# Kernel optimization log

Measured on AMD Instinct MI355X. Metric: run time of the kernel, lower is better.

The kernel has to match this reference:

```python
import jax, jax.numpy as jnp
import numpy as np

DIM = 1024
HEADS = 16
HEAD_DIM = DIM // HEADS
FFN = 4 * DIM
EPS = 1e-5


def layer_norm(x, g, b):
    mu = jnp.mean(x, axis=-1, keepdims=True)
    var = jnp.mean(jnp.square(x - mu), axis=-1, keepdims=True)
    return (x - mu) * jax.lax.rsqrt(var + EPS) * g + b


def setup_inputs() -> dict:
    key = jax.random.key(0)
    ks = jax.random.split(key, 12)
    s_d = 1.0 / np.sqrt(DIM)
    s_f = 1.0 / np.sqrt(FFN)
    return {
        "x": jax.random.normal(ks[0], (2, 2048, DIM), dtype=jnp.float32),
        "ln1_g": jnp.ones((DIM,), jnp.float32),
        "ln1_b": jnp.zeros((DIM,), jnp.float32),
        "q_w": jax.random.normal(ks[1], (DIM, DIM), jnp.float32) * s_d,
        "k_w": jax.random.normal(ks[2], (DIM, DIM), jnp.float32) * s_d,
        "v_w": jax.random.normal(ks[3], (DIM, DIM), jnp.float32) * s_d,
        "o_w": jax.random.normal(ks[4], (DIM, DIM), jnp.float32) * s_d,
        "ln2_g": jnp.ones((DIM,), jnp.float32),
        "ln2_b": jnp.zeros((DIM,), jnp.float32),
        "ffn_in_w": jax.random.normal(ks[5], (FFN, DIM), jnp.float32) * s_d,
        "ffn_in_b": jnp.zeros((FFN,), jnp.float32),
        "sw_w": jax.random.normal(ks[6], (FFN, FFN), jnp.float32) * s_f,
        "sw_v": jax.random.normal(ks[7], (FFN, FFN), jnp.float32) * s_f,
        "ffn_out_w": jax.random.normal(ks[8], (DIM, FFN), jnp.float32) * s_f,
        "ffn_out_b": jnp.zeros((DIM,), jnp.float32),
    }


def reference(x, ln1_g, ln1_b, q_w, k_w, v_w, o_w, ln2_g, ln2_b,
              ffn_in_w, ffn_in_b, sw_w, sw_v, ffn_out_w, ffn_out_b):
    B, L, D = x.shape
    scale = HEAD_DIM ** -0.5

    # --- attention block ---
    h = layer_norm(x, ln1_g, ln1_b)
    q = (h @ q_w.T).reshape(B, L, HEADS, HEAD_DIM).transpose(0, 2, 1, 3)
    k = (h @ k_w.T).reshape(B, L, HEADS, HEAD_DIM).transpose(0, 2, 1, 3)
    v = (h @ v_w.T).reshape(B, L, HEADS, HEAD_DIM).transpose(0, 2, 1, 3)
    attn = jnp.einsum("bhqd,bhkd->bhqk", q, k) * scale
    attn = jax.nn.softmax(attn, axis=-1)
    out = jnp.einsum("bhqk,bhkd->bhqd", attn, v)
    out = out.transpose(0, 2, 1, 3).reshape(B, L, D)
    x = x + out @ o_w.T

    # --- FFN block: Linear -> SwiGLU -> Linear ---
    h = layer_norm(x, ln2_g, ln2_b)
    u = h @ ffn_in_w.T + ffn_in_b                 # [B,L,FFN]
    g = jax.nn.silu(u @ sw_w.T) * (u @ sw_v.T)    # SwiGLU
    x = x + g @ ffn_out_w.T + ffn_out_b
    return x
```

## Files before the change

kernel.cpp:

```cpp
#include <hip/hip_runtime.h>
#include <hip/hip_bf16.h>

#define TOK 4096
#define DIM 1024
#define FFN_N 4096
#define SEQ 2048
#define HD 64
#define QKS 3072

using short8 = __attribute__((ext_vector_type(8))) short;
using short4v = __attribute__((ext_vector_type(4))) short;
using f32x4 = __attribute__((ext_vector_type(4))) float;

__device__ __forceinline__ short f2b(float f){
  return __builtin_bit_cast(short, __float2bfloat16(f));
}
__device__ __forceinline__ float b2f(short s){
  return __bfloat162float(__builtin_bit_cast(__hip_bfloat16, s));
}
__device__ __forceinline__ unsigned cvtpk(float lo, float hi){
  unsigned r;
  asm("v_cvt_pk_bf16_f32 %0, %1, %2" : "=v"(r) : "v"(lo), "v"(hi));
  return r;
}

__device__ __forceinline__ void gl_lds16(const short* g, short* l){
  __builtin_amdgcn_global_load_lds(
      (const __attribute__((address_space(1))) unsigned int*)g,
      (__attribute__((address_space(3))) unsigned int*)l, 16, 0, 0);
}

#define BARRAW() asm volatile("s_barrier" ::: "memory")
#define VMCNT(n) asm volatile("s_waitcnt vmcnt(" #n ")" ::: "memory")

__global__ __launch_bounds__(256) void castk(const float* __restrict__ src,
                                             short* __restrict__ dst, int n){
  int stride = gridDim.x*256*4;
  for (int i = (blockIdx.x*256 + threadIdx.x)*4; i < n; i += stride){
    float4 v = *reinterpret_cast<const float4*>(src + i);
    short4v o; o[0]=f2b(v.x); o[1]=f2b(v.y); o[2]=f2b(v.z); o[3]=f2b(v.w);
    *reinterpret_cast<short4v*>(dst + i) = o;
  }
}

__global__ __launch_bounds__(256) void lnk(const float* __restrict__ x,
                                           const float* __restrict__ g,
                                           const float* __restrict__ b,
                                           short* __restrict__ out){
  int row = blockIdx.x;
  int t = threadIdx.x;
  const float* xr = x + (size_t)row*DIM;
  float4 v = *reinterpret_cast<const float4*>(xr + t*4);
  float s = v.x+v.y+v.z+v.w;
  float s2 = v.x*v.x+v.y*v.y+v.z*v.z+v.w*v.w;
  #pragma unroll
  for (int off=1; off<64; off<<=1){ s += __shfl_xor(s,off); s2 += __shfl_xor(s2,off); }
  __shared__ float as_[4], as2_[4];
  if ((t&63)==0){ as_[t>>6]=s; as2_[t>>6]=s2; }
  __syncthreads();
  s = as_[0]+as_[1]+as_[2]+as_[3];
  s2 = as2_[0]+as2_[1]+as2_[2]+as2_[3];
  float mu = s * (1.0f/DIM);
  float var = s2 * (1.0f/DIM) - mu*mu;
  float r = rsqrtf(var + 1e-5f);
  float4 gv = *reinterpret_cast<const float4*>(g + t*4);
  float4 bv = *reinterpret_cast<const float4*>(b + t*4);
  short4v o;
  o[0]=f2b((v.x-mu)*r*gv.x + bv.x);
  o[1]=f2b((v.y-mu)*r*gv.y + bv.y);
  o[2]=f2b((v.z-mu)*r*gv.z + bv.z);
  o[3]=f2b((v.w-mu)*r*gv.w + bv.w);
  *reinterpret_cast<short4v*>(out + (size_t)row*DIM + t*4) = o;
}

template<int MODE>
__global__ __launch_bounds__(256,2) void gemm_bt(
    const short* __restrict__ A, const short* __restrict__ Bt,
    short* __restrict__ Cb, float* __restrict__ Cf,
    const float* __restrict__ bias, const float* __restrict__ resid,
    const short* __restrict__ aux,
    int M, int N, int K)
{
  __shared__ __align__(16) short Al[128*32];
  __shared__ __align__(16) short Bl[128*32];
  const int tid = threadIdx.x, lane = tid & 63, w = tid >> 6;
  const int wr = w >> 1, wc = w & 1;
  const int bx = blockIdx.x, by = blockIdx.y;

  const short* ga0 = A  + (size_t)(by*128 + w*32 + (lane>>2))*K + (lane&3)*8;
  const short* gb0 = Bt + (size_t)(bx*128 + w*32 + (lane>>2))*K + (lane&3)*8;
  short* la0 = &Al[w*32*32];
  short* lb0 = &Bl[w*32*32];

  f32x4 acc[4][4] = {};

  for (int k0 = 0; k0 < K; k0 += 32){
    __syncthreads();
    gl_lds16(ga0 + k0,                 la0);
    gl_lds16(ga0 + k0 + (size_t)16*K,  la0 + 16*32);
    gl_lds16(gb0 + k0,                 lb0);
    gl_lds16(gb0 + k0 + (size_t)16*K,  lb0 + 16*32);
    __syncthreads();
    short8 af[4], bf[4];
    #pragma unroll
    for (int m=0;m<4;m++)
      af[m] = *reinterpret_cast<const short8*>(&Al[(wr*64 + m*16 + (lane&15))*32 + (lane>>4)*8]);
    #pragma unroll
    for (int n=0;n<4;n++)
      bf[n] = *reinterpret_cast<const short8*>(&Bl[(wc*64 + n*16 + (lane&15))*32 + (lane>>4)*8]);
    #pragma unroll
    for (int m=0;m<4;m++)
      #pragma unroll
      for (int n=0;n<4;n++)
        acc[m][n] = __builtin_amdgcn_mfma_f32_16x16x32_bf16(af[m], bf[n], acc[m][n], 0,0,0);
  }

  #pragma unroll
  for (int m=0;m<4;m++){
    #pragma unroll
    for (int n=0;n<4;n++){
      #pragma unroll
      for (int j=0;j<4;j++){
        int r = by*128 + wr*64 + m*16 + ((lane>>4)<<2) + j;
        int c = bx*128 + wc*64 + n*16 + (lane&15);
        float v = acc[m][n][j];
        if (MODE==1 || MODE==3) v += bias[c];
        size_t idx = (size_t)r*N + c;
        if (MODE==4){
          float a = b2f(aux[idx]);
          float sg = a / (1.0f + __expf(-a));
          Cb[idx] = f2b(sg * v);
        } else if (MODE<=1) {
          Cb[idx] = f2b(v);
        } else {
          Cf[idx] = resid[idx] + v;
        }
      }
    }
  }
}

template<int MODE>
__global__ __launch_bounds__(512,2) void gemm256(
    const short* __restrict__ A, const short* __restrict__ Bt,
    short* __restrict__ Cb,
    const float* __restrict__ bias, const short* __restrict__ aux,
    int M, int N, int K)
{
  __shared__ __align__(16) short L[65536];
  const int tid = threadIdx.x, lane = tid&63, w = tid>>6;
  const int q15 = lane&15, h8 = lane>>4;
  const int wm = w>>2, wn = w&3;
  const int NT = K>>6;

  int bid = blockIdx.x;
  int wg = (bid&7)*(gridDim.x>>3) + (bid>>3);
  const int by = wg >> 4, bx = wg & 15;

  const int isub = w*8 + (lane>>3);
  const int koff = ((lane&7) ^ ((lane>>3)&7))*8;

  const short* gA[2][2]; const short* gB[2][2];
  #pragma unroll
  for (int hh=0; hh<2; hh++){
    #pragma unroll
    for (int j=0; j<2; j++){
      int i = j*64 + isub;
      int Ra = by*256 + (i>>6)*128 + hh*64 + (i&63);
      gA[hh][j] = A + (size_t)Ra*K + koff;
      int Rb = bx*256 + (i>>5)*64 + hh*32 + (i&31);
      gB[hh][j] = Bt + (size_t)Rb*K + koff;
    }
  }

  auto stA = [&](int db, int hh, int j, int kt){
    gl_lds16(gA[hh][j] + (size_t)kt*64, &L[db*32768 + hh*8192 + j*4096 + w*512]);
  };
  auto stB = [&](int db, int hh, int j, int kt){
    gl_lds16(gB[hh][j] + (size_t)kt*64, &L[db*32768 + (2+hh)*8192 + j*4096 + w*512]);
  };
  auto rdA = [&](int db, int mh, int m, int ks)->short8{
    int i = wm*64 + m*16 + q15;
    int ch = (ks*4 + h8) ^ (i&7);
    return *reinterpret_cast<const short8*>(&L[db*32768 + mh*8192 + i*64 + ch*8]);
  };
  auto rdB = [&](int db, int nh, int n, int ks)->short8{
    int i = wn*32 + n*16 + q15;
    int ch = (ks*4 + h8) ^ (i&7);
    return *reinterpret_cast<const short8*>(&L[db*32768 + (2+nh)*8192 + i*64 + ch*8]);
  };

  f32x4 acc[8][4] = {};
  short8 af[4][2], bf0[2][2], bf1[2][2];

#define MFMA_QUAD(MH, NH, BF)                                                  \
  __builtin_amdgcn_s_setprio(1);                                               \
  _Pragma("unroll")                                                            \
  for (int m=0;m<4;m++){                                                       \
    _Pragma("unroll")                                                          \
    for (int n=0;n<2;n++){                                                     \
      acc[(MH)*4+m][(NH)*2+n] = __builtin_amdgcn_mfma_f32_16x16x32_bf16(       \
          af[m][0], BF[n][0], acc[(MH)*4+m][(NH)*2+n], 0,0,0);                 \
      acc[(MH)*4+m][(NH)*2+n] = __builtin_amdgcn_mfma_f32_16x16x32_bf16(       \
          af[m][1], BF[n][1], acc[(MH)*4+m][(NH)*2+n], 0,0,0);                 \
    }                                                                          \
  }                                                                            \
  __builtin_amdgcn_s_setprio(0);

  stA(0,0,0,0); stA(0,0,1,0);
  stB(0,0,0,0); stB(0,0,1,0);
  stA(0,1,0,0); stA(0,1,1,0);
  stB(0,1,0,0); stB(0,1,1,0);
  VMCNT(4);
  BARRAW();

  for (int t = 0; t < NT; ++t){
    const int db = t&1;
    const bool pf = (t+1 < NT);

    #pragma unroll
    for (int m=0;m<4;m++){ af[m][0]=rdA(db,0,m,0); af[m][1]=rdA(db,0,m,1); }
    #pragma unroll
    for (int n=0;n<2;n++){ bf0[n][0]=rdB(db,0,n,0); bf0[n][1]=rdB(db,0,n,1); }
    if (pf){ stA(db^1,0,0,t+1); stA(db^1,0,1,t+1);
             stB(db^1,0,0,t+1); stB(db^1,0,1,t+1); }
    MFMA_QUAD(0,0,bf0);

    if (pf){ VMCNT(4); } else { VMCNT(0); }
    BARRAW();

    #pragma unroll
    for (int n=0;n<2;n++){ bf1[n][0]=rdB(db,1,n,0); bf1[n][1]=rdB(db,1,n,1); }
    if (pf){ stA(db^1,1,0,t+1); stA(db^1,1,1,t+1);
             stB(db^1,1,0,t+1); stB(db^1,1,1,t+1); }
    MFMA_QUAD(0,1,bf1);

    #pragma unroll
    for (int m=0;m<4;m++){ af[m][0]=rdA(db,1,m,0); af[m][1]=rdA(db,1,m,1); }
    MFMA_QUAD(1,1,bf1);
    MFMA_QUAD(1,0,bf0);

    if (pf){ VMCNT(4); }
    BARRAW();
  }

  #pragma unroll
  for (int mq=0;mq<8;mq++){
    #pragma unroll
    for (int nq=0;nq<4;nq++){
      #pragma unroll
      for (int jj=0;jj<4;jj++){
        int r = by*256 + wm*128 + mq*16 + h8*4 + jj;
        int c = bx*256 + wn*64  + nq*16 + q15;
        float v = acc[mq][nq][jj];
        if (MODE==1) v += bias[c];
        size_t idx = (size_t)r*N + c;
        if (MODE==4){
          float a = b2f(aux[idx]);
          float sg = a / (1.0f + __expf(-a));
          Cb[idx] = f2b(sg * v);
        } else {
          Cb[idx] = f2b(v);
        }
      }
    }
  }
#undef MFMA_QUAD
}

__global__ __launch_bounds__(256) void vtrk(const short* __restrict__ V,
                                            short* __restrict__ Vt){
  __shared__ __align__(16) short T[64*72];
  const int tid = threadIdx.x;
  const int bh = blockIdx.y;
  const int b = bh >> 4, hd = bh & 15;
  const int t0 = blockIdx.x * 64;
  const short* src = V + (size_t)b*SEQ*QKS + (size_t)hd*HD;

  const int r = tid>>2, c = tid&3;
  short8 a0 = *reinterpret_cast<const short8*>(src + (size_t)(t0+r)*QKS + c*8);
  short8 a1 = *reinterpret_cast<const short8*>(src + (size_t)(t0+r)*QKS + (c+4)*8);
  *reinterpret_cast<short8*>(&T[r*72 + c*8]) = a0;
  *reinterpret_cast<short8*>(&T[r*72 + (c+4)*8]) = a1;
  __syncthreads();

  short* dst = Vt + (size_t)bh*HD*SEQ;
  #pragma unroll
  for (int dd=0; dd<2; dd++){
    int d = (tid>>3) + dd*32;
    int tc = tid&7;
    short8 o;
    #pragma unroll
    for (int j=0;j<8;j++) o[j] = T[(tc*8+j)*72 + d];
    *reinterpret_cast<short8*>(dst + (size_t)d*SEQ + t0 + tc*8) = o;
  }
}

__global__ __launch_bounds__(256) void attnk(
    const short* __restrict__ Q, const short* __restrict__ K,
    const short* __restrict__ Vt, short* __restrict__ O)
{
  __shared__ __align__(16) short Kl[64*64];
  __shared__ __align__(16) short Vl[64*64];
  __shared__ __align__(16) short Pl[4*16*72];

  const int tid = threadIdx.x, lane = tid&63, w = tid>>6;
  const int h = lane>>4, q15 = lane&15;
  const int bh = blockIdx.y;
  const int b = bh >> 4, hd = bh & 15;
  const int q0 = blockIdx.x * 64;
  const size_t base  = (size_t)b*SEQ*QKS + (size_t)hd*HD;
  const size_t obase = (size_t)b*SEQ*DIM + (size_t)hd*HD;
  const size_t vbase = (size_t)bh*HD*SEQ;

  short8 aq[2];
  {
    int qrow = q0 + w*16 + q15;
    const short* qp = Q + base + (size_t)qrow*QKS + h*8;
    aq[0] = *reinterpret_cast<const short8*>(qp);
    aq[1] = *reinterpret_cast<const short8*>(qp + 32);
  }

  float mrun = -1e30f, lrun = 0.f;
  f32x4 o[4] = {};

  const int ksub = lane>>3;
  const int kchunk = (lane&7) ^ ksub;
  const short* kg0 = K + base + (size_t)(w*16 + ksub)*QKS + kchunk*8;
  const short* kg1 = kg0 + (size_t)8*QKS;
  const short* vg0 = Vt + vbase + (size_t)(w*16 + ksub)*SEQ + kchunk*8;
  const short* vg1 = vg0 + (size_t)8*SEQ;
  short* kl0 = &Kl[(w*16)*64];
  short* kl1 = &Kl[(w*16 + 8)*64];
  short* vl0 = &Vl[(w*16)*64];
  short* vl1 = &Vl[(w*16 + 8)*64];

  short* plw = &Pl[w*16*72];
  const int xk = (q15&7);

  for (int kv0 = 0; kv0 < SEQ; kv0 += 64){
    __syncthreads();
    gl_lds16(kg0 + (size_t)kv0*QKS, kl0);
    gl_lds16(kg1 + (size_t)kv0*QKS, kl1);
    gl_lds16(vg0 + kv0, vl0);
    gl_lds16(vg1 + kv0, vl1);
    __syncthreads();

    f32x4 s[4];
    #pragma unroll
    for (int nt=0; nt<4; nt++){
      const short8 kf0 = *reinterpret_cast<const short8*>(
          &Kl[(nt*16+q15)*64 + ((h    ^ xk)*8)]);
      const short8 kf1 = *reinterpret_cast<const short8*>(
          &Kl[(nt*16+q15)*64 + (((4+h)^ xk)*8)]);
      f32x4 t = {};
      t = __builtin_amdgcn_mfma_f32_16x16x32_bf16(kf0, aq[0], t, 0,0,0);
      t = __builtin_amdgcn_mfma_f32_16x16x32_bf16(kf1, aq[1], t, 0,0,0);
      s[nt] = t * 0.125f;
    }

    float pm = s[0][0];
    #pragma unroll
    for (int nt=0; nt<4; nt++)
      #pragma unroll
      for (int j=0; j<4; j++) pm = fmaxf(pm, s[nt][j]);
    pm = fmaxf(pm, __shfl_xor(pm, 16));
    pm = fmaxf(pm, __shfl_xor(pm, 32));

    float mn = fmaxf(mrun, pm);
    float al = __expf(mrun - mn);
    mrun = mn;
    float rs = 0.f;
    #pragma unroll
    for (int nt=0; nt<4; nt++)
      #pragma unroll
      for (int j=0; j<4; j++){
        s[nt][j] = __expf(s[nt][j] - mn);
        rs += s[nt][j];
      }
    rs += __shfl_xor(rs, 16);
    rs += __shfl_xor(rs, 32);
    lrun = lrun*al + rs;

    float alj[4];
    #pragma unroll
    for (int j=0;j<4;j++) alj[j] = __shfl(al, 4*h + j);
    #pragma unroll
    for (int dt=0;dt<4;dt++)
      #pragma unroll
      for (int j=0;j<4;j++) o[dt][j] *= alj[j];

    #pragma unroll
    for (int nt=0;nt<4;nt++){
      uint2 u;
      u.x = cvtpk(s[nt][0], s[nt][1]);
      u.y = cvtpk(s[nt][2], s[nt][3]);
      *reinterpret_cast<uint2*>(&plw[q15*72 + nt*16 + 4*h]) = u;
    }
    asm volatile("s_waitcnt lgkmcnt(0)" ::: "memory");
    const short8 ap0 = *reinterpret_cast<const short8*>(&plw[q15*72 +      h*8]);
    const short8 ap1 = *reinterpret_cast<const short8*>(&plw[q15*72 + 32 + h*8]);

    #pragma unroll
    for (int dt=0;dt<4;dt++){
      const short8 vf0 = *reinterpret_cast<const short8*>(
          &Vl[(dt*16+q15)*64 + ((h    ^ xk)*8)]);
      const short8 vf1 = *reinterpret_cast<const short8*>(
          &Vl[(dt*16+q15)*64 + (((4+h)^ xk)*8)]);
      o[dt] = __builtin_amdgcn_mfma_f32_16x16x32_bf16(ap0, vf0, o[dt], 0,0,0);
      o[dt] = __builtin_amdgcn_mfma_f32_16x16x32_bf16(ap1, vf1, o[dt], 0,0,0);
    }
  }

  float rl[4];
  #pragma unroll
  for (int j=0;j<4;j++) rl[j] = 1.0f / __shfl(lrun, 4*h + j);
  #pragma unroll
  for (int dt=0;dt<4;dt++)
    #pragma unroll
    for (int j=0;j<4;j++){
      int qrow = q0 + w*16 + 4*h + j;
      O[obase + (size_t)qrow*DIM + dt*16 + q15] = f2b(o[dt][j]*rl[j]);
    }
}

extern "C" void kernel_launch(void* const* d_in, const int* in_sizes, int n_in,
                              void* d_out, int out_size, void* d_ws, size_t ws_size,
                              hipStream_t stream) {
  const float* x     = (const float*)d_in[0];
  const float* ln1_g = (const float*)d_in[1];
  const float* ln1_b = (const float*)d_in[2];
  const float* q_w   = (const float*)d_in[3];
  const float* k_w   = (const float*)d_in[4];
  const float* v_w   = (const float*)d_in[5];
  const float* o_w   = (const float*)d_in[6];
  const float* ln2_g = (const float*)d_in[7];
  const float* ln2_b = (const float*)d_in[8];
  const float* fi_w  = (const float*)d_in[9];
  const float* fi_b  = (const float*)d_in[10];
  const float* sw_w  = (const float*)d_in[11];
  const float* sw_v  = (const float*)d_in[12];
  const float* fo_w  = (const float*)d_in[13];
  const float* fo_b  = (const float*)d_in[14];
  float* out = (float*)d_out;

  char* W = (char*)d_ws;
  const size_t MB = 1024*1024;
  short* qkvw = (short*)(W +   0*MB);
  short* ow   = (short*)(W +   6*MB);
  short* fiw  = (short*)(W +   8*MB);
  short* sww  = (short*)(W +  16*MB);
  short* swv  = (short*)(W +  48*MB);
  short* fow  = (short*)(W +  80*MB);
  short* hb   = (short*)(W +  88*MB);
  short* qkv  = (short*)(W +  96*MB);
  short* ab   = (short*)(W + 120*MB);
  float* x2   = (float*)(W + 128*MB);
  short* ub   = (short*)(W + 144*MB);
  short* gb   = (short*)(W + 176*MB);
  short* a1   = (short*)(W +  96*MB);
  short* vt   = (short*)(W + 144*MB);

  dim3 blk(256);
  castk<<<1024,blk,0,stream>>>(q_w, qkvw,             1024*1024);
  castk<<<1024,blk,0,stream>>>(k_w, qkvw + 1024*1024, 1024*1024);
  castk<<<1024,blk,0,stream>>>(v_w, qkvw + 2048*1024, 1024*1024);
  castk<<<1024,blk,0,stream>>>(o_w, ow, 1024*1024);
  castk<<<2048,blk,0,stream>>>(fi_w, fiw, 4096*1024);
  castk<<<2048,blk,0,stream>>>(sw_w, sww, 4096*4096);
  castk<<<2048,blk,0,stream>>>(sw_v, swv, 4096*4096);
  castk<<<2048,blk,0,stream>>>(fo_w, fow, 1024*4096);

  lnk<<<TOK,blk,0,stream>>>(x, ln1_g, ln1_b, hb);
  gemm_bt<0><<<dim3(24,32),blk,0,stream>>>(hb, qkvw, qkv, nullptr, nullptr, nullptr, nullptr, TOK, QKS, DIM);
  vtrk<<<dim3(SEQ/64,32),blk,0,stream>>>(qkv + 2048, vt);
  attnk<<<dim3(32,32),blk,0,stream>>>(qkv, qkv + 1024, vt, ab);
  gemm_bt<2><<<dim3(8,32),blk,0,stream>>>(ab, ow, nullptr, x2, nullptr, x, nullptr, TOK, DIM, DIM);
  lnk<<<TOK,blk,0,stream>>>(x2, ln2_g, ln2_b, hb);
  gemm256<1><<<256, 512, 0, stream>>>(hb, fiw, ub, fi_b, nullptr, TOK, FFN_N, DIM);
  gemm256<0><<<256, 512, 0, stream>>>(ub, sww, a1, nullptr, nullptr, TOK, FFN_N, FFN_N);
  gemm256<4><<<256, 512, 0, stream>>>(ub, swv, gb, nullptr, a1, TOK, FFN_N, FFN_N);
  gemm_bt<3><<<dim3(8,32),blk,0,stream>>>(gb, fow, nullptr, out, fo_b, x2, nullptr, TOK, DIM, FFN_N);
}
```

Measured before the change: 574.4 us.

## Double-buffer K/V tiles in attention with 128-key blocks and prefetch

The attention kernel now loads 128-key K/V tiles into double-buffered LDS and prefetches the next tile while computing the current one, which halves the barrier count per key. The V transpose kernel writes its output pre-swizzled so the direct global-to-LDS copy lands in the layout the MFMA reads expect. The aim is to hide global load latency behind MFMA and softmax work. In exchange, LDS use grows to about 64KB per block, which may cut occupancy.

```diff
diff --git a/kernel.cpp b/kernel.cpp
--- a/kernel.cpp
+++ b/kernel.cpp
@@ -292,16 +292,16 @@
     short8 o;
     #pragma unroll
     for (int j=0;j<8;j++) o[j] = T[(tc*8+j)*72 + d];
-    *reinterpret_cast<short8*>(dst + (size_t)d*SEQ + t0 + tc*8) = o;
+    *reinterpret_cast<short8*>(dst + (size_t)d*SEQ + t0 + ((tc ^ (d&7))*8)) = o;
   }
 }
 
 __global__ __launch_bounds__(256) void attnk(
     const short* __restrict__ Q, const short* __restrict__ K,
-    const short* __restrict__ Vt, short* __restrict__ O)
+    const short* __restrict__ Vp, short* __restrict__ O)
 {
-  __shared__ __align__(16) short Kl[64*64];
-  __shared__ __align__(16) short Vl[64*64];
+  __shared__ __align__(16) short Kb[2][128*64];
+  __shared__ __align__(16) short Vb[2][64*128];
   __shared__ __align__(16) short Pl[4*16*72];
 
   const int tid = threadIdx.x, lane = tid&63, w = tid>>6;
@@ -324,92 +324,104 @@
   float mrun = -1e30f, lrun = 0.f;
   f32x4 o[4] = {};
 
-  const int ksub = lane>>3;
-  const int kchunk = (lane&7) ^ ksub;
-  const short* kg0 = K + base + (size_t)(w*16 + ksub)*QKS + kchunk*8;
-  const short* kg1 = kg0 + (size_t)8*QKS;
-  const short* vg0 = Vt + vbase + (size_t)(w*16 + ksub)*SEQ + kchunk*8;
-  const short* vg1 = vg0 + (size_t)8*SEQ;
-  short* kl0 = &Kl[(w*16)*64];
-  short* kl1 = &Kl[(w*16 + 8)*64];
-  short* vl0 = &Vl[(w*16)*64];
-  short* vl1 = &Vl[(w*16 + 8)*64];
+  const short* kgp0 = K + base + (size_t)(w*32 + (lane>>3))*QKS
+                        + ((lane&7) ^ ((lane>>3)&7))*8;
+  const short* vgp0 = Vp + vbase + (size_t)(w*16 + (lane>>4))*SEQ + (lane&15)*8;
 
   short* plw = &Pl[w*16*72];
   const int xk = (q15&7);
 
-  for (int kv0 = 0; kv0 < SEQ; kv0 += 64){
-    __syncthreads();
-    gl_lds16(kg0 + (size_t)kv0*QKS, kl0);
-    gl_lds16(kg1 + (size_t)kv0*QKS, kl1);
-    gl_lds16(vg0 + kv0, vl0);
-    gl_lds16(vg1 + kv0, vl1);
-    __syncthreads();
-
-    f32x4 s[4];
-    #pragma unroll
-    for (int nt=0; nt<4; nt++){
-      const short8 kf0 = *reinterpret_cast<const short8*>(
-          &Kl[(nt*16+q15)*64 + ((h    ^ xk)*8)]);
-      const short8 kf1 = *reinterpret_cast<const short8*>(
-          &Kl[(nt*16+q15)*64 + (((4+h)^ xk)*8)]);
-      f32x4 t = {};
-      t = __builtin_amdgcn_mfma_f32_16x16x32_bf16(kf0, aq[0], t, 0,0,0);
-      t = __builtin_amdgcn_mfma_f32_16x16x32_bf16(kf1, aq[1], t, 0,0,0);
-      s[nt] = t * 0.125f;
-    }
-
-    float pm = s[0][0];
-    #pragma unroll
-    for (int nt=0; nt<4; nt++)
-      #pragma unroll
-      for (int j=0; j<4; j++) pm = fmaxf(pm, s[nt][j]);
-    pm = fmaxf(pm, __shfl_xor(pm, 16));
-    pm = fmaxf(pm, __shfl_xor(pm, 32));
-
-    float mn = fmaxf(mrun, pm);
-    float al = __expf(mrun - mn);
-    mrun = mn;
-    float rs = 0.f;
-    #pragma unroll
-    for (int nt=0; nt<4; nt++)
-      #pragma unroll
-      for (int j=0; j<4; j++){
-        s[nt][j] = __expf(s[nt][j] - mn);
-        rs += s[nt][j];
+  #pragma unroll
+  for (int i=0;i<4;i++) gl_lds16(kgp0 + (size_t)(i*8)*QKS, &Kb[0][(w*32 + i*8)*64]);
+  #pragma unroll
+  for (int i=0;i<4;i++) gl_lds16(vgp0 + (size_t)(i*4)*SEQ, &Vb[0][(w*16 + i*4)*128]);
+  VMCNT(0);
+  BARRAW();
+
+  int db = 0;
+  for (int kv0 = 0; kv0 < SEQ; kv0 += 128){
+    const bool pf = (kv0 + 128 < SEQ);
+    if (pf){
+      #pragma unroll
+      for (int i=0;i<4;i++)
+        gl_lds16(kgp0 + (size_t)(kv0 + 128 + i*8)*QKS, &Kb[db^1][(w*32 + i*8)*64]);
+      #pragma unroll
+      for (int i=0;i<4;i++)
+        gl_lds16(vgp0 + (size_t)(i*4)*SEQ + (kv0 + 128), &Vb[db^1][(w*16 + i*4)*128]);
+    }
+
+    #pragma unroll
+    for (int sub=0; sub<2; sub++){
+      const short* Kl = &Kb[db][sub*64*64];
+      f32x4 s[4];
+      #pragma unroll
+      for (int nt=0; nt<4; nt++){
+        const short8 kf0 = *reinterpret_cast<const short8*>(
+            &Kl[(nt*16+q15)*64 + ((h    ^ xk)*8)]);
+        const short8 kf1 = *reinterpret_cast<const short8*>(
+            &Kl[(nt*16+q15)*64 + (((4+h)^ xk)*8)]);
+        f32x4 t = {};
+        t = __builtin_amdgcn_mfma_f32_16x16x32_bf16(kf0, aq[0], t, 0,0,0);
+        t = __builtin_amdgcn_mfma_f32_16x16x32_bf16(kf1, aq[1], t, 0,0,0);
+        s[nt] = t * 0.125f;
       }
-    rs += __shfl_xor(rs, 16);
-    rs += __shfl_xor(rs, 32);
-    lrun = lrun*al + rs;
-
-    float alj[4];
-    #pragma unroll
-    for (int j=0;j<4;j++) alj[j] = __shfl(al, 4*h + j);
-    #pragma unroll
-    for (int dt=0;dt<4;dt++)
-      #pragma unroll
-      for (int j=0;j<4;j++) o[dt][j] *= alj[j];
-
-    #pragma unroll
-    for (int nt=0;nt<4;nt++){
-      uint2 u;
-      u.x = cvtpk(s[nt][0], s[nt][1]);
-      u.y = cvtpk(s[nt][2], s[nt][3]);
-      *reinterpret_cast<uint2*>(&plw[q15*72 + nt*16 + 4*h]) = u;
-    }
-    asm volatile("s_waitcnt lgkmcnt(0)" ::: "memory");
-    const short8 ap0 = *reinterpret_cast<const short8*>(&plw[q15*72 +      h*8]);
-    const short8 ap1 = *reinterpret_cast<const short8*>(&plw[q15*72 + 32 + h*8]);
-
-    #pragma unroll
-    for (int dt=0;dt<4;dt++){
-      const short8 vf0 = *reinterpret_cast<const short8*>(
-          &Vl[(dt*16+q15)*64 + ((h    ^ xk)*8)]);
-      const short8 vf1 = *reinterpret_cast<const short8*>(
-          &Vl[(dt*16+q15)*64 + (((4+h)^ xk)*8)]);
-      o[dt] = __builtin_amdgcn_mfma_f32_16x16x32_bf16(ap0, vf0, o[dt], 0,0,0);
-      o[dt] = __builtin_amdgcn_mfma_f32_16x16x32_bf16(ap1, vf1, o[dt], 0,0,0);
-    }
+
+      float pm = s[0][0];
+      #pragma unroll
+      for (int nt=0; nt<4; nt++)
+        #pragma unroll
+        for (int j=0; j<4; j++) pm = fmaxf(pm, s[nt][j]);
+      pm = fmaxf(pm, __shfl_xor(pm, 16));
+      pm = fmaxf(pm, __shfl_xor(pm, 32));
+
+      float mn = fmaxf(mrun, pm);
+      float al = __expf(mrun - mn);
+      mrun = mn;
+      float rs = 0.f;
+      #pragma unroll
+      for (int nt=0; nt<4; nt++)
+        #pragma unroll
+        for (int j=0; j<4; j++){
+          s[nt][j] = __expf(s[nt][j] - mn);
+          rs += s[nt][j];
+        }
+      rs += __shfl_xor(rs, 16);
+      rs += __shfl_xor(rs, 32);
+      lrun = lrun*al + rs;
+
+      float alj[4];
+      #pragma unroll
+      for (int j=0;j<4;j++) alj[j] = __shfl(al, 4*h + j);
+      #pragma unroll
+      for (int dt=0;dt<4;dt++)
+        #pragma unroll
+        for (int j=0;j<4;j++) o[dt][j] *= alj[j];
+
+      #pragma unroll
+      for (int nt=0;nt<4;nt++){
+        uint2 u;
+        u.x = cvtpk(s[nt][0], s[nt][1]);
+        u.y = cvtpk(s[nt][2], s[nt][3]);
+        *reinterpret_cast<uint2*>(&plw[q15*72 + nt*16 + 4*h]) = u;
+      }
+      asm volatile("s_waitcnt lgkmcnt(0)" ::: "memory");
+      const short8 ap0 = *reinterpret_cast<const short8*>(&plw[q15*72 +      h*8]);
+      const short8 ap1 = *reinterpret_cast<const short8*>(&plw[q15*72 + 32 + h*8]);
+
+      #pragma unroll
+      for (int dt=0;dt<4;dt++){
+        const short8 vf0 = *reinterpret_cast<const short8*>(
+            &Vb[db][(dt*16+q15)*128 + sub*64 + ((h    ^ xk)*8)]);
+        const short8 vf1 = *reinterpret_cast<const short8*>(
+            &Vb[db][(dt*16+q15)*128 + sub*64 + (((4+h)^ xk)*8)]);
+        o[dt] = __builtin_amdgcn_mfma_f32_16x16x32_bf16(ap0, vf0, o[dt], 0,0,0);
+        o[dt] = __builtin_amdgcn_mfma_f32_16x16x32_bf16(ap1, vf1, o[dt], 0,0,0);
+      }
+    }
+
+    if (pf){ VMCNT(0); }
+    BARRAW();
+    db ^= 1;
   }
 
   float rl[4];
```

Result: no change. 585.1 us (+1.9%).
